# Optimization experiments

Measured on AMD Instinct MI355X. Metric: run time of the kernel, lower is better.

Reference implementation:

```python
import jax, jax.numpy as jnp
import numpy as np

DIM = 1024
NUM_HEADS = 16
HEAD_DIM = DIM // NUM_HEADS
MLP_DIM = 4 * DIM
EPS = 1e-5


def layer_norm(x, g, b):
    mu = jnp.mean(x, axis=-1, keepdims=True)
    var = jnp.mean(jnp.square(x - mu), axis=-1, keepdims=True)
    return (x - mu) * jax.lax.rsqrt(var + EPS) * g + b


def setup_inputs() -> dict:
    key = jax.random.key(0)
    ks = jax.random.split(key, 12)
    B, L = 2, 2048
    s = lambda n: 1.0 / np.sqrt(n)
    return {
        "x": jax.random.normal(ks[0], (B, L, DIM), jnp.float32),
        "attn_mask": jnp.tril(jnp.ones((L, L), jnp.int32))[None, None],  # [1,1,L,L]
        "w_qkv": jax.random.normal(ks[1], (DIM, 3 * DIM), jnp.float32) * s(DIM),
        "b_qkv": jnp.zeros((3 * DIM,), jnp.float32),
        "w_proj": jax.random.normal(ks[2], (DIM, DIM), jnp.float32) * s(DIM),
        "b_proj": jnp.zeros((DIM,), jnp.float32),
        "w_fc1": jax.random.normal(ks[3], (DIM, MLP_DIM), jnp.float32) * s(DIM),
        "b_fc1": jnp.zeros((MLP_DIM,), jnp.float32),
        "w_fc2": jax.random.normal(ks[4], (MLP_DIM, DIM), jnp.float32) * s(MLP_DIM),
        "b_fc2": jnp.zeros((DIM,), jnp.float32),
        "g1": jnp.ones((DIM,), jnp.float32),
        "beta1": jnp.zeros((DIM,), jnp.float32),
        "g2": jnp.ones((DIM,), jnp.float32),
        "beta2": jnp.zeros((DIM,), jnp.float32),
    }


def reference(x, attn_mask, w_qkv, b_qkv, w_proj, b_proj, w_fc1, b_fc1,
              w_fc2, b_fc2, g1, beta1, g2, beta2):
    B, L, D = x.shape
    scale = HEAD_DIM ** -0.5

    # --- attention branch (pre-norm) ---
    h = layer_norm(x, g1, beta1)
    qkv = h @ w_qkv + b_qkv                                  # [B,L,3D]
    qkv = qkv.reshape(B, L, 3, NUM_HEADS, HEAD_DIM)
    q = qkv[:, :, 0].transpose(0, 2, 1, 3)                   # [B,H,L,hd]
    k = qkv[:, :, 1].transpose(0, 2, 1, 3)
    v = qkv[:, :, 2].transpose(0, 2, 1, 3)
    attn = jnp.einsum('bhqd,bhkd->bhqk', q, k) * scale       # [B,H,L,L]
    attn = jnp.where(attn_mask == 0, -jnp.inf, attn)
    attn = jax.nn.softmax(attn, axis=-1)
    y = jnp.einsum('bhqk,bhkd->bhqd', attn, v)               # [B,H,L,hd]
    y = y.transpose(0, 2, 1, 3).reshape(B, L, D)
    y = y @ w_proj + b_proj
    x = x + y

    # --- MLP branch (pre-norm) ---
    h = layer_norm(x, g2, beta2)
    h = jax.nn.gelu(h @ w_fc1 + b_fc1, approximate=False)
    h = h @ w_fc2 + b_fc2
    return x + h
```

## Files before the change

kernel.cpp:

```cpp
#include <hip/hip_runtime.h>
#include <hip/hip_bf16.h>
#include <stdint.h>

typedef unsigned short u16;
typedef __attribute__((ext_vector_type(8))) short bf16x8;
typedef __attribute__((ext_vector_type(4))) short bf16x4;
typedef __attribute__((ext_vector_type(4))) float f32x4;
typedef __attribute__((ext_vector_type(16))) float f32x16;
typedef __attribute__((ext_vector_type(4))) unsigned short u16x4;

#define DEVI static __device__ __forceinline__

DEVI u16 f2bf(float f) {
    unsigned int u = __builtin_bit_cast(unsigned int, f);
    return (u16)((u + 0x7fffu + ((u >> 16) & 1u)) >> 16);
}

DEVI float bf2f(u16 v) { return __builtin_bit_cast(float, ((unsigned)v) << 16); }

DEVI float4 ldbf4(const u16* p, size_t idx4) {
    const u16x4 v = ((const u16x4*)p)[idx4];
    float4 o;
    o.x = bf2f(v[0]); o.y = bf2f(v[1]); o.z = bf2f(v[2]); o.w = bf2f(v[3]);
    return o;
}

DEVI float gelu_f(float v) {
    const float z = 1.5957691216f * (v + 0.044715f * v * v * v);
    return v / (1.0f + __expf(-z));
}

DEVI void async_copy16(const void* g, void* l) {
    __builtin_amdgcn_global_load_lds((const __attribute__((address_space(1))) void*)g,
                                     (__attribute__((address_space(3))) void*)l,
                                     16, 0, 0);
}

__global__ __launch_bounds__(256) void prep_kernel(const float* __restrict__ wq, u16* __restrict__ dq,
                                                   const float* __restrict__ wp, u16* __restrict__ dp,
                                                   const float* __restrict__ w1, u16* __restrict__ d1,
                                                   const float* __restrict__ w2, u16* __restrict__ d2,
                                                   const float* __restrict__ x,
                                                   const float* __restrict__ g1,
                                                   const float* __restrict__ be1,
                                                   u16* __restrict__ ln1out) {
    __shared__ float tile[32][33];
    __shared__ float red[8];
    const int id = blockIdx.x;
    const int t = threadIdx.x;
    if (id >= 12288) {
        const int row = id - 12288;
        const float4 v = ((const float4*)(x + (size_t)row * 1024))[t];
        float s  = v.x + v.y + v.z + v.w;
        float ss = v.x * v.x + v.y * v.y + v.z * v.z + v.w * v.w;
#pragma unroll
        for (int off = 32; off > 0; off >>= 1) {
            s  += __shfl_down(s, off);
            ss += __shfl_down(ss, off);
        }
        const int wv = t >> 6;
        if ((t & 63) == 0) { red[wv] = s; red[4 + wv] = ss; }
        __syncthreads();
        if (t == 0) {
            red[0] = red[0] + red[1] + red[2] + red[3];
            red[4] = red[4] + red[5] + red[6] + red[7];
        }
        __syncthreads();
        const float mean = red[0] * (1.0f / 1024.0f);
        const float var  = red[4] * (1.0f / 1024.0f) - mean * mean;
        const float rstd = rsqrtf(var + 1e-5f);
        const float4 gv = ((const float4*)g1)[t];
        const float4 bv = ((const float4*)be1)[t];
        u16x4 o;
        o[0] = f2bf((v.x - mean) * rstd * gv.x + bv.x);
        o[1] = f2bf((v.y - mean) * rstd * gv.y + bv.y);
        o[2] = f2bf((v.z - mean) * rstd * gv.z + bv.z);
        o[3] = f2bf((v.w - mean) * rstd * gv.w + bv.w);
        ((u16x4*)ln1out)[(size_t)row * 256 + t] = o;
        return;
    }
    const float* src; u16* dst; int K, N, k0, n0;
    if (id < 3072)      {               src = wq; dst = dq; K = 1024; N = 3072; k0 = (id & 31) << 5; n0 = (id >> 5) << 5; }
    else if (id < 4096) { int l = id - 3072; src = wp; dst = dp; K = 1024; N = 1024; k0 = (l & 31) << 5; n0 = (l >> 5) << 5; }
    else if (id < 8192) { int l = id - 4096; src = w1; dst = d1; K = 1024; N = 4096; k0 = (l & 31) << 5; n0 = (l >> 5) << 5; }
    else                { int l = id - 8192; src = w2; dst = d2; K = 4096; N = 1024; k0 = (l & 127) << 5; n0 = (l >> 7) << 5; }
    const int c = t & 31, r0 = t >> 5;
#pragma unroll
    for (int p = 0; p < 4; ++p) {
        const int r = r0 + p * 8;
        tile[r][c] = src[(size_t)(k0 + r) * N + n0 + c];
    }
    __syncthreads();
#pragma unroll
    for (int p = 0; p < 4; ++p) {
        const int r = r0 + p * 8;
        dst[(size_t)(n0 + r) * K + k0 + c] = f2bf(tile[c][r]);
    }
}

DEVI void stage64(const char* g, size_t ldb, char* lds0, int lane, int wv) {
    const int colsw = ((lane & 3) << 4) ^ (lane & 32);
    const int rl = lane >> 2;
#pragma unroll
    for (int i = 0; i < 4; ++i) {
        const int s = wv * 4 + i;
        const int kh = s >> 3, c = s & 7;
        async_copy16(g + (size_t)(c * 16 + rl) * ldb + kh * 64 + colsw,
                     lds0 + s * 1024);
    }
}

template <int EPI, int SPLITK>
__global__ __launch_bounds__(256, 4) void gemmv6(const u16* __restrict__ A,
                                                 const u16* __restrict__ Bt,
                                                 const float* __restrict__ bias,
                                                 void* __restrict__ out0,
                                                 void* __restrict__ out1,
                                                 void* __restrict__ out2,
                                                 int M, int N, int K) {
    __shared__ __align__(16) char As[16384];
    __shared__ __align__(16) char Bs[16384];
    const int tid = threadIdx.x;
    const int lane = tid & 63, wv = tid >> 6;
    const int wr = wv >> 1, wc = wv & 1;
    const int g = lane >> 4, qq = lane & 15;
    const int rdoff = qq * 64 + ((g * 16) ^ ((qq & 8) << 2));

    const int nwg = gridDim.x;
    int id = blockIdx.x;
    id = (id & 7) * (nwg >> 3) + (id >> 3);
    const int MT = M >> 7, NTn = N >> 7;
    const int slice = id / (MT * NTn);
    const int r2 = id % (MT * NTn);
    const int m0 = (r2 % MT) << 7;
    const int n0 = (r2 / MT) << 7;
    const int Ks = K / SPLITK;
    const int NT = Ks >> 6;
    const size_t ldb = (size_t)K * 2;

    const char* pa = (const char*)A + (size_t)m0 * ldb + (size_t)slice * Ks * 2;
    const char* pb = (const char*)Bt + (size_t)n0 * ldb + (size_t)slice * Ks * 2;

    f32x4 acc[4][4] = {};

    for (int t = 0; t < NT; ++t) {
        stage64(pa + (size_t)t * 128, ldb, As, lane, wv);
        stage64(pb + (size_t)t * 128, ldb, Bs, lane, wv);
        __syncthreads();
#pragma unroll
        for (int kh = 0; kh < 2; ++kh) {
            bf16x8 fa[4], fb[4];
#pragma unroll
            for (int fn = 0; fn < 4; ++fn)
                fb[fn] = *(const bf16x8*)(Bs + (kh * 8 + wc * 4 + fn) * 1024 + rdoff);
#pragma unroll
            for (int fm = 0; fm < 4; ++fm)
                fa[fm] = *(const bf16x8*)(As + (kh * 8 + wr * 4 + fm) * 1024 + rdoff);
#pragma unroll
            for (int fm = 0; fm < 4; ++fm)
#pragma unroll
                for (int fn = 0; fn < 4; ++fn)
                    acc[fm][fn] = __builtin_amdgcn_mfma_f32_16x16x32_bf16(fa[fm], fb[fn],
                                                                          acc[fm][fn], 0, 0, 0);
        }
        __syncthreads();
    }

#pragma unroll
    for (int fm = 0; fm < 4; ++fm) {
#pragma unroll
        for (int fn = 0; fn < 4; ++fn) {
            const int mrow = m0 + wr * 64 + fm * 16 + g * 4;
            const int ncol = n0 + wc * 64 + fn * 16 + qq;
            if constexpr (EPI == 0) {
                const float bs = bias[ncol];
                const int sec = ncol >> 10;
                const int hd_ = ncol & 1023;
                const int hh = hd_ >> 6, dd = hd_ & 63;
                if (sec == 2) {
                    const int b_ = mrow >> 11, l_ = mrow & 2047;
                    u16x4 pk;
#pragma unroll
                    for (int r = 0; r < 4; ++r) pk[r] = f2bf(acc[fm][fn][r] + bs);
                    *(u16x4*)((u16*)out2 + ((size_t)((b_ * 16 + hh) * 64 + dd)) * 2048 + l_) = pk;
                } else {
                    u16* dst = (sec == 0) ? (u16*)out0 : (u16*)out1;
                    const float sc = (sec == 0) ? 0.1803368801f : 1.0f;
#pragma unroll
                    for (int r = 0; r < 4; ++r) {
                        const int mr = mrow + r;
                        const int b_ = mr >> 11, l_ = mr & 2047;
                        dst[((size_t)((b_ * 16 + hh) * 2048 + l_)) * 64 + dd] =
                            f2bf((acc[fm][fn][r] + bs) * sc);
                    }
                }
            } else if constexpr (EPI == 2) {
                const float bs = bias[ncol];
                u16* dst = (u16*)out0;
#pragma unroll
                for (int r = 0; r < 4; ++r)
                    dst[(size_t)(mrow + r) * N + ncol] = f2bf(gelu_f(acc[fm][fn][r] + bs));
            } else {
                u16* dst = (u16*)out0 + (size_t)slice * M * N;
#pragma unroll
                for (int r = 0; r < 4; ++r)
                    dst[(size_t)(mrow + r) * N + ncol] = f2bf(acc[fm][fn][r]);
            }
        }
    }
}

template <int SPLIT>
__global__ __launch_bounds__(256) void reduceN_kernel(const u16* __restrict__ p,
                                                      const float* __restrict__ bias,
                                                      const float* __restrict__ res,
                                                      float* __restrict__ out,
                                                      int MN4, int N4) {
    const int i = blockIdx.x * 256 + threadIdx.x;
    float4 s = ldbf4(p, i);
#pragma unroll
    for (int s2 = 1; s2 < SPLIT; ++s2) {
        const float4 q = ldbf4(p, (size_t)s2 * MN4 + i);
        s.x += q.x; s.y += q.y; s.z += q.z; s.w += q.w;
    }
    const float4 r = ((const float4*)res)[i];
    const float4 bs = ((const float4*)bias)[i & (N4 - 1)];
    float4 o;
    o.x = s.x + r.x + bs.x;
    o.y = s.y + r.y + bs.y;
    o.z = s.z + r.z + bs.z;
    o.w = s.w + r.w + bs.w;
    ((float4*)out)[i] = o;
}

template <int SPLIT>
__global__ __launch_bounds__(256) void reduceLN_kernel(const u16* __restrict__ p,
                                                       const float* __restrict__ bias,
                                                       const float* __restrict__ res,
                                                       const float* __restrict__ gw,
                                                       const float* __restrict__ bw,
                                                       float* __restrict__ xout,
                                                       u16* __restrict__ lnout,
                                                       int MN4) {
    const int row = blockIdx.x;
    const int t = threadIdx.x;
    const int i = row * 256 + t;
    float4 s = ldbf4(p, i);
#pragma unroll
    for (int s2 = 1; s2 < SPLIT; ++s2) {
        const float4 q = ldbf4(p, (size_t)s2 * MN4 + i);
        s.x += q.x; s.y += q.y; s.z += q.z; s.w += q.w;
    }
    const float4 r = ((const float4*)res)[i];
    const float4 bs = ((const float4*)bias)[t];
    float4 o;
    o.x = s.x + r.x + bs.x;
    o.y = s.y + r.y + bs.y;
    o.z = s.z + r.z + bs.z;
    o.w = s.w + r.w + bs.w;
    ((float4*)xout)[i] = o;
    float sum  = o.x + o.y + o.z + o.w;
    float ssum = o.x * o.x + o.y * o.y + o.z * o.z + o.w * o.w;
#pragma unroll
    for (int off = 32; off > 0; off >>= 1) {
        sum  += __shfl_down(sum, off);
        ssum += __shfl_down(ssum, off);
    }
    __shared__ float red[8];
    const int wv = t >> 6;
    if ((t & 63) == 0) { red[wv] = sum; red[4 + wv] = ssum; }
    __syncthreads();
    if (t == 0) {
        red[0] = red[0] + red[1] + red[2] + red[3];
        red[4] = red[4] + red[5] + red[6] + red[7];
    }
    __syncthreads();
    const float mean = red[0] * (1.0f / 1024.0f);
    const float var  = red[4] * (1.0f / 1024.0f) - mean * mean;
    const float rstd = rsqrtf(var + 1e-5f);
    const float4 gv = ((const float4*)gw)[t];
    const float4 bv = ((const float4*)bw)[t];
    u16x4 ov;
    ov[0] = f2bf((o.x - mean) * rstd * gv.x + bv.x);
    ov[1] = f2bf((o.y - mean) * rstd * gv.y + bv.y);
    ov[2] = f2bf((o.z - mean) * rstd * gv.z + bv.z);
    ov[3] = f2bf((o.w - mean) * rstd * gv.w + bv.w);
    ((u16x4*)lnout)[(size_t)row * 256 + t] = ov;
}

DEVI void stage_kv2(const char* kbase, const char* vbase, int key0,
                    u16* ksm, u16* vsm, int wv, int lane) {
#pragma unroll
    for (int i = 0; i < 2; ++i) {
        const int c = wv + i * 4;
        const int off = c * 1024 + lane * 16;
        const int row = off >> 7;
        const int scol = (off & 127) ^ ((row & 7) << 4);
        async_copy16(kbase + (size_t)key0 * 128 + (size_t)row * 128 + scol,
                     (char*)ksm + c * 1024);
    }
#pragma unroll
    for (int i = 0; i < 2; ++i) {
        const int c = wv + i * 4;
        const int row = c * 8 + (lane >> 3);
        const int scol = ((lane & 7) * 16) ^ ((row & 7) << 4);
        async_copy16(vbase + (size_t)row * 4096 + (size_t)key0 * 2 + scol,
                     (char*)vsm + c * 1024);
    }
}

__global__ __launch_bounds__(256, 3) void attn32_kernel(const u16* __restrict__ Q,
                                                        const u16* __restrict__ Kk,
                                                        const u16* __restrict__ Vt,
                                                        u16* __restrict__ Y) {
    const int id = blockIdx.x;
    const int bh = id & 31;
    const int qb = 15 - (id >> 5);
    const int b_ = bh >> 4, hh = bh & 15;
    const int tid = threadIdx.x;
    const int wv = tid >> 6, lane = tid & 63;
    const int hi = lane >> 5, qc = lane & 31;

    __shared__ __align__(16) u16 Ksm[2][4096];
    __shared__ __align__(16) u16 Vsm[2][4096];
    __shared__ __align__(16) u16 Pl[4][32 * 68];

    const char* Kb = (const char*)(Kk + (size_t)bh * 2048 * 64);
    const char* Vb = (const char*)(Vt + (size_t)bh * 64 * 2048);
    u16* Pw = &Pl[wv][0];

    const int q0w = qb * 128 + wv * 32;
    const int qg = q0w + qc;
    const int ntile = qb * 2 + 2;
    const int ntile_w = qb * 2 + (wv >> 1) + 1;

    bf16x8 qf[4];
    {
        const u16* Qp = Q + ((size_t)bh * 2048 + qg) * 64;
#pragma unroll
        for (int c = 0; c < 4; ++c)
            qf[c] = *(const bf16x8*)(Qp + c * 16 + hi * 8);
    }

    f32x16 oacc[2];
#pragma unroll
    for (int r = 0; r < 16; ++r) { oacc[0][r] = 0.0f; oacc[1][r] = 0.0f; }
    float m_run = -60000.0f, l_run = 0.0f;

    stage_kv2(Kb, Vb, 0, Ksm[0], Vsm[0], wv, lane);
    __syncthreads();
    int cur = 0;
    for (int kt = 0; kt < ntile; ++kt) {
        const int key0 = kt * 64;
        if (kt + 1 < ntile)
            stage_kv2(Kb, Vb, key0 + 64, Ksm[cur ^ 1], Vsm[cur ^ 1], wv, lane);
        if (kt < ntile_w) {
            f32x16 sacc[2];
#pragma unroll
            for (int r = 0; r < 16; ++r) { sacc[0][r] = 0.0f; sacc[1][r] = 0.0f; }
#pragma unroll
            for (int c = 0; c < 4; ++c) {
#pragma unroll
                for (int kb = 0; kb < 2; ++kb) {
                    const int kr = kb * 32 + qc;
                    const bf16x8 ak = *(const bf16x8*)((const char*)Ksm[cur] + kr * 128 +
                                          ((c * 32 + hi * 16) ^ ((kr & 7) << 4)));
                    sacc[kb] = __builtin_amdgcn_mfma_f32_32x32x16_bf16(ak, qf[c],
                                                                       sacc[kb], 0, 0, 0);
                }
            }
            float pmax = -1e30f;
            if (key0 + 63 > q0w) {
#pragma unroll
                for (int kb = 0; kb < 2; ++kb)
#pragma unroll
                    for (int r = 0; r < 16; ++r) {
                        const int key = key0 + kb * 32 + (r & 3) + 8 * (r >> 2) + 4 * hi;
                        float s = sacc[kb][r];
                        if (key > qg) s = -1e30f;
                        sacc[kb][r] = s;
                        pmax = fmaxf(pmax, s);
                    }
            } else {
#pragma unroll
                for (int kb = 0; kb < 2; ++kb)
#pragma unroll
                    for (int r = 0; r < 16; ++r) pmax = fmaxf(pmax, sacc[kb][r]);
            }
            pmax = fmaxf(pmax, __shfl_xor(pmax, 32));
            if (pmax > m_run + 11.0f) {
                const float alpha = __builtin_amdgcn_exp2f(m_run - pmax);
#pragma unroll
                for (int r = 0; r < 16; ++r) { oacc[0][r] *= alpha; oacc[1][r] *= alpha; }
                l_run *= alpha;
                m_run = pmax;
            }
            float lsum = 0.0f;
#pragma unroll
            for (int kb = 0; kb < 2; ++kb)
#pragma unroll
                for (int j = 0; j < 4; ++j) {
                    u16x4 pk4;
#pragma unroll
                    for (int t = 0; t < 4; ++t) {
                        const float e = __builtin_amdgcn_exp2f(sacc[kb][j * 4 + t] - m_run);
                        lsum += e;
                        pk4[t] = f2bf(e);
                    }
                    *(u16x4*)(Pw + qc * 68 + kb * 32 + j * 8 + 4 * hi) = pk4;
                }
            lsum += __shfl_xor(lsum, 32);
            l_run += lsum;
#pragma unroll
            for (int c = 0; c < 4; ++c) {
                const u16* pp = Pw + qc * 68 + c * 16 + hi * 8;
                union { bf16x8 v; struct { bf16x4 lo; bf16x4 hi2; } s; } u;
                u.s.lo  = *(const bf16x4*)(pp);
                u.s.hi2 = *(const bf16x4*)(pp + 4);
                const bf16x8 pf = u.v;
#pragma unroll
                for (int db = 0; db < 2; ++db) {
                    const int dr = db * 32 + qc;
                    const bf16x8 av = *(const bf16x8*)((const char*)Vsm[cur] + dr * 128 +
                                          ((c * 32 + hi * 16) ^ ((dr & 7) << 4)));
                    oacc[db] = __builtin_amdgcn_mfma_f32_32x32x16_bf16(av, pf,
                                                                       oacc[db], 0, 0, 0);
                }
            }
        }
        __syncthreads();
        cur ^= 1;
    }
    const float inv = 1.0f / l_run;
    u16* Yp = &Y[((size_t)(b_ * 2048 + qg)) * 1024 + hh * 64];
#pragma unroll
    for (int db = 0; db < 2; ++db)
#pragma unroll
        for (int j = 0; j < 4; ++j) {
            u16x4 o;
#pragma unroll
            for (int t = 0; t < 4; ++t) o[t] = f2bf(oacc[db][j * 4 + t] * inv);
            *(u16x4*)(Yp + db * 32 + j * 8 + 4 * hi) = o;
        }
}

extern "C" void kernel_launch(void* const* d_in, const int* in_sizes, int n_in,
                              void* d_out, int out_size, void* d_ws, size_t ws_size,
                              hipStream_t stream) {
    (void)in_sizes; (void)n_in; (void)out_size;
    const float* x      = (const float*)d_in[0];
    const float* w_qkv  = (const float*)d_in[2];
    const float* b_qkv  = (const float*)d_in[3];
    const float* w_proj = (const float*)d_in[4];
    const float* b_proj = (const float*)d_in[5];
    const float* w_fc1  = (const float*)d_in[6];
    const float* b_fc1  = (const float*)d_in[7];
    const float* w_fc2  = (const float*)d_in[8];
    const float* b_fc2  = (const float*)d_in[9];
    const float* g1     = (const float*)d_in[10];
    const float* be1    = (const float*)d_in[11];
    const float* g2     = (const float*)d_in[12];
    const float* be2    = (const float*)d_in[13];

    char* ws = (char*)d_ws;
    size_t off = 0;
    auto alloc = [&](size_t bytes) { size_t r = off; off += (bytes + 255) & ~(size_t)255; return r; };
    u16*   wt_qkv = (u16*)(ws + alloc((size_t)3072 * 1024 * 2));
    u16*   wt_prj = (u16*)(ws + alloc((size_t)1024 * 1024 * 2));
    u16*   wt_fc1 = (u16*)(ws + alloc((size_t)4096 * 1024 * 2));
    u16*   wt_fc2 = (u16*)(ws + alloc((size_t)1024 * 4096 * 2));
    u16*   hbuf   = (u16*)(ws + alloc((size_t)4096 * 1024 * 2));
    float* x1     = (float*)(ws + alloc((size_t)4096 * 1024 * 4));
    char*  big    = ws + alloc((size_t)33554432);
    u16* qb  = (u16*)(big);
    u16* kb  = (u16*)(big + 8388608);
    u16* vtb = (u16*)(big + 16777216);
    u16* yb  = (u16*)(big + 25165824);
    u16* act = (u16*)(big);
    if (off > ws_size) return;
    const size_t part_need = (size_t)4 * 4096 * 1024 * 2;
    if ((ws_size - off) < part_need) return;
    u16* part = (u16*)(ws + off);

    const dim3 blk(256);
    prep_kernel<<<dim3(16384), blk, 0, stream>>>(w_qkv, wt_qkv, w_proj, wt_prj,
                                                 w_fc1, wt_fc1, w_fc2, wt_fc2,
                                                 x, g1, be1, hbuf);
    gemmv6<0, 1><<<dim3(768), blk, 0, stream>>>(hbuf, wt_qkv, b_qkv,
                                                qb, kb, vtb, 4096, 3072, 1024);
    attn32_kernel<<<dim3(512), blk, 0, stream>>>(qb, kb, vtb, yb);
    gemmv6<5, 2><<<dim3(512), blk, 0, stream>>>(yb, wt_prj, nullptr,
                                                part, nullptr, nullptr, 4096, 1024, 1024);
    reduceLN_kernel<2><<<dim3(4096), blk, 0, stream>>>(part, b_proj, x, g2, be2,
                                                       x1, hbuf, 1048576);
    gemmv6<2, 1><<<dim3(1024), blk, 0, stream>>>(hbuf, wt_fc1, b_fc1,
                                                 act, nullptr, nullptr, 4096, 4096, 1024);
    gemmv6<5, 4><<<dim3(1024), blk, 0, stream>>>(act, wt_fc2, nullptr,
                                                 part, nullptr, nullptr, 4096, 1024, 4096);
    reduceN_kernel<4><<<dim3(4096), blk, 0, stream>>>(part, b_fc2, x1, (float*)d_out,
                                                      1048576, 256);
}
```

Before: 220.8 us.

## Split causal attention over two key segments and merge with a combine kernel

The attention kernel now splits each query block's key range into two halves, running them as separate workgroups (1024 blocks instead of 512). Each block writes unnormalized bf16 partial outputs plus per-row max and sum, and a new combine kernel merges them into Y. The K/V double buffering is replaced by single-buffered staging with smaller shared memory, allowing 4 blocks per CU. The P buffer is shrunk and the PV MFMAs are interleaved per 32-key chunk. This is meant to fix load imbalance and low parallelism from causal masking. In exchange it adds an extra kernel, partial-output traffic, bf16 rounding of the unnormalized partials, and loses copy/compute overlap.

```diff
diff --git a/kernel.cpp b/kernel.cpp
--- a/kernel.cpp
+++ b/kernel.cpp
@@ -288,7 +288,7 @@
     ((u16x4*)lnout)[(size_t)row * 256 + t] = ov;
 }
 
-DEVI void stage_kv2(const char* kbase, const char* vbase, int key0,
+DEVI void stage_kv1(const char* kbase, const char* vbase, int key0,
                     u16* ksm, u16* vsm, int wv, int lane) {
 #pragma unroll
     for (int i = 0; i < 2; ++i) {
@@ -309,30 +309,34 @@
     }
 }
 
-__global__ __launch_bounds__(256, 3) void attn32_kernel(const u16* __restrict__ Q,
-                                                        const u16* __restrict__ Kk,
-                                                        const u16* __restrict__ Vt,
-                                                        u16* __restrict__ Y) {
+__global__ __launch_bounds__(256, 4) void attn32_seg(const u16* __restrict__ Q,
+                                                     const u16* __restrict__ Kk,
+                                                     const u16* __restrict__ Vt,
+                                                     u16* __restrict__ opart,
+                                                     float2* __restrict__ ml) {
     const int id = blockIdx.x;
     const int bh = id & 31;
-    const int qb = 15 - (id >> 5);
-    const int b_ = bh >> 4, hh = bh & 15;
+    const int seg = (id >> 5) & 1;
+    const int qb = 15 - (id >> 6);
     const int tid = threadIdx.x;
     const int wv = tid >> 6, lane = tid & 63;
     const int hi = lane >> 5, qc = lane & 31;
 
-    __shared__ __align__(16) u16 Ksm[2][4096];
-    __shared__ __align__(16) u16 Vsm[2][4096];
-    __shared__ __align__(16) u16 Pl[4][32 * 68];
+    __shared__ __align__(16) u16 Ksm[4096];
+    __shared__ __align__(16) u16 Vsm[4096];
+    __shared__ __align__(16) u16 Pl[4][32 * 36];
 
     const char* Kb = (const char*)(Kk + (size_t)bh * 2048 * 64);
     const char* Vb = (const char*)(Vt + (size_t)bh * 64 * 2048);
     u16* Pw = &Pl[wv][0];
+    const u16* Pr = Pw + qc * 36;
 
     const int q0w = qb * 128 + wv * 32;
     const int qg = q0w + qc;
-    const int ntile = qb * 2 + 2;
-    const int ntile_w = qb * 2 + (wv >> 1) + 1;
+    const int nt_half = qb + 1;
+    const int kt_begin = seg ? nt_half : 0;
+    const int kt_end = seg ? (2 * qb + 2) : nt_half;
+    const int ntw = min(kt_end, 2 * qb + (wv >> 1) + 1);
 
     bf16x8 qf[4];
     {
@@ -347,14 +351,11 @@
     for (int r = 0; r < 16; ++r) { oacc[0][r] = 0.0f; oacc[1][r] = 0.0f; }
     float m_run = -60000.0f, l_run = 0.0f;
 
-    stage_kv2(Kb, Vb, 0, Ksm[0], Vsm[0], wv, lane);
-    __syncthreads();
-    int cur = 0;
-    for (int kt = 0; kt < ntile; ++kt) {
+    for (int kt = kt_begin; kt < kt_end; ++kt) {
         const int key0 = kt * 64;
-        if (kt + 1 < ntile)
-            stage_kv2(Kb, Vb, key0 + 64, Ksm[cur ^ 1], Vsm[cur ^ 1], wv, lane);
-        if (kt < ntile_w) {
+        stage_kv1(Kb, Vb, key0, Ksm, Vsm, wv, lane);
+        __syncthreads();
+        if (kt < ntw) {
             f32x16 sacc[2];
 #pragma unroll
             for (int r = 0; r < 16; ++r) { sacc[0][r] = 0.0f; sacc[1][r] = 0.0f; }
@@ -363,7 +364,7 @@
 #pragma unroll
                 for (int kb = 0; kb < 2; ++kb) {
                     const int kr = kb * 32 + qc;
-                    const bf16x8 ak = *(const bf16x8*)((const char*)Ksm[cur] + kr * 128 +
+                    const bf16x8 ak = *(const bf16x8*)((const char*)Ksm + kr * 128 +
                                           ((c * 32 + hi * 16) ^ ((kr & 7) << 4)));
                     sacc[kb] = __builtin_amdgcn_mfma_f32_32x32x16_bf16(ak, qf[c],
                                                                        sacc[kb], 0, 0, 0);
@@ -397,7 +398,7 @@
             }
             float lsum = 0.0f;
 #pragma unroll
-            for (int kb = 0; kb < 2; ++kb)
+            for (int kb = 0; kb < 2; ++kb) {
 #pragma unroll
                 for (int j = 0; j < 4; ++j) {
                     u16x4 pk4;
@@ -407,41 +408,63 @@
                         lsum += e;
                         pk4[t] = f2bf(e);
                     }
-                    *(u16x4*)(Pw + qc * 68 + kb * 32 + j * 8 + 4 * hi) = pk4;
+                    *(u16x4*)(Pw + qc * 36 + j * 8 + 4 * hi) = pk4;
                 }
+#pragma unroll
+                for (int s = 0; s < 2; ++s) {
+                    const int c = kb * 2 + s;
+                    const bf16x8 pf = *(const bf16x8*)(Pr + s * 16 + hi * 8);
+#pragma unroll
+                    for (int db = 0; db < 2; ++db) {
+                        const int dr = db * 32 + qc;
+                        const bf16x8 av = *(const bf16x8*)((const char*)Vsm + dr * 128 +
+                                              ((c * 32 + hi * 16) ^ ((dr & 7) << 4)));
+                        oacc[db] = __builtin_amdgcn_mfma_f32_32x32x16_bf16(av, pf,
+                                                                           oacc[db], 0, 0, 0);
+                    }
+                }
+            }
             lsum += __shfl_xor(lsum, 32);
             l_run += lsum;
-#pragma unroll
-            for (int c = 0; c < 4; ++c) {
-                const u16* pp = Pw + qc * 68 + c * 16 + hi * 8;
-                union { bf16x8 v; struct { bf16x4 lo; bf16x4 hi2; } s; } u;
-                u.s.lo  = *(const bf16x4*)(pp);
-                u.s.hi2 = *(const bf16x4*)(pp + 4);
-                const bf16x8 pf = u.v;
-#pragma unroll
-                for (int db = 0; db < 2; ++db) {
-                    const int dr = db * 32 + qc;
-                    const bf16x8 av = *(const bf16x8*)((const char*)Vsm[cur] + dr * 128 +
-                                          ((c * 32 + hi * 16) ^ ((dr & 7) << 4)));
-                    oacc[db] = __builtin_amdgcn_mfma_f32_32x32x16_bf16(av, pf,
-                                                                       oacc[db], 0, 0, 0);
-                }
-            }
         }
         __syncthreads();
-        cur ^= 1;
-    }
-    const float inv = 1.0f / l_run;
-    u16* Yp = &Y[((size_t)(b_ * 2048 + qg)) * 1024 + hh * 64];
+    }
+
+    const size_t row = (size_t)seg * 65536 + (size_t)bh * 2048 + qg;
+    u16* op = opart + row * 64;
 #pragma unroll
     for (int db = 0; db < 2; ++db)
 #pragma unroll
         for (int j = 0; j < 4; ++j) {
             u16x4 o;
 #pragma unroll
-            for (int t = 0; t < 4; ++t) o[t] = f2bf(oacc[db][j * 4 + t] * inv);
-            *(u16x4*)(Yp + db * 32 + j * 8 + 4 * hi) = o;
+            for (int t = 0; t < 4; ++t) o[t] = f2bf(oacc[db][j * 4 + t]);
+            *(u16x4*)(op + db * 32 + j * 8 + 4 * hi) = o;
         }
+    if (hi == 0) { float2 t2; t2.x = m_run; t2.y = l_run; ml[row] = t2; }
+}
+
+__global__ __launch_bounds__(256) void attn_comb2(const u16* __restrict__ opart,
+                                                  const float2* __restrict__ ml,
+                                                  u16* __restrict__ Y) {
+    const int idx = blockIdx.x * 256 + threadIdx.x;
+    const int row = idx >> 4, d4 = idx & 15;
+    const float2 ml0 = ml[row];
+    const float2 ml1 = ml[65536 + row];
+    const float m = fmaxf(ml0.x, ml1.x);
+    const float w0 = __builtin_amdgcn_exp2f(ml0.x - m);
+    const float w1 = __builtin_amdgcn_exp2f(ml1.x - m);
+    const float inv = 1.0f / (ml0.y * w0 + ml1.y * w1);
+    const float4 a = ldbf4(opart, (size_t)row * 16 + d4);
+    const float4 b = ldbf4(opart, (size_t)(65536 + row) * 16 + d4);
+    const int bh = row >> 11, q = row & 2047;
+    const int b_ = bh >> 4, hh = bh & 15;
+    u16x4 o;
+    o[0] = f2bf((a.x * w0 + b.x * w1) * inv);
+    o[1] = f2bf((a.y * w0 + b.y * w1) * inv);
+    o[2] = f2bf((a.z * w0 + b.z * w1) * inv);
+    o[3] = f2bf((a.w * w0 + b.w * w1) * inv);
+    *(u16x4*)(Y + ((size_t)(b_ * 2048 + q)) * 1024 + hh * 64 + d4 * 4) = o;
 }
 
 extern "C" void kernel_launch(void* const* d_in, const int* in_sizes, int n_in,
@@ -481,6 +504,8 @@
     const size_t part_need = (size_t)4 * 4096 * 1024 * 2;
     if ((ws_size - off) < part_need) return;
     u16* part = (u16*)(ws + off);
+    u16* opart = part;
+    float2* mlp = (float2*)(ws + off + (size_t)2 * 65536 * 64 * 2);
 
     const dim3 blk(256);
     prep_kernel<<<dim3(16384), blk, 0, stream>>>(w_qkv, wt_qkv, w_proj, wt_prj,
@@ -488,7 +513,8 @@
                                                  x, g1, be1, hbuf);
     gemmv6<0, 1><<<dim3(768), blk, 0, stream>>>(hbuf, wt_qkv, b_qkv,
                                                 qb, kb, vtb, 4096, 3072, 1024);
-    attn32_kernel<<<dim3(512), blk, 0, stream>>>(qb, kb, vtb, yb);
+    attn32_seg<<<dim3(1024), blk, 0, stream>>>(qb, kb, vtb, opart, mlp);
+    attn_comb2<<<dim3(4096), blk, 0, stream>>>(opart, mlp, yb);
     gemmv6<5, 2><<<dim3(512), blk, 0, stream>>>(yb, wt_prj, nullptr,
                                                 part, nullptr, nullptr, 4096, 1024, 1024);
     reduceLN_kernel<2><<<dim3(4096), blk, 0, stream>>>(part, b_proj, x, g2, be2,
```

Result: no change. 221.1 us (+0.1%).
